# Kernel optimization log

Hardware: AMD Instinct MI355X
Metric: run time of the kernel (lower is better)

The kernel has to match this reference:

```python
import jax, jax.numpy as jnp
import numpy as np

N = 100000   # nodes (batched molecular graphs)
E = 400000   # directed edges
D = 300      # hidden_dim (GNN default)
L = 3        # depth


def setup_inputs() -> dict:
    key = jax.random.key(0)
    ks = jax.random.split(key, 32)
    w = lambda k, s: (jax.random.normal(k, s, dtype=jnp.float32) * 0.05)
    inp = {
        "x": jax.random.normal(ks[0], (N, D), dtype=jnp.float32),
        "edge_attr": jax.random.normal(ks[1], (E, D), dtype=jnp.float32),
        "edge_index": jax.random.randint(ks[2], (2, E), 0, N),
        "W_edge": w(ks[3], (L, D, D)), "b_edge": w(ks[4], (L, D)),
        "W_in":  w(ks[5], (L, D, D)),  # node_in Linear, bias=False
        "W_out": w(ks[6], (L, D, D)),  # node_out Linear, bias=False
        "W_em1": w(ks[7], (L, D, D)),  "b_em1": w(ks[8], (L, D)),
        "W_em2": w(ks[9], (L, D, D)),  "b_em2": w(ks[10], (L, D)),
        "W_n1a": w(ks[11], (L, D, D)), "b_n1a": w(ks[12], (L, D)),
        "W_n1b": w(ks[13], (L, D, D)), "b_n1b": w(ks[14], (L, D)),
        "W_n2a": w(ks[15], (L, D, D)), "b_n2a": w(ks[16], (L, D)),
        "W_n2b": w(ks[17], (L, D, D)), "b_n2b": w(ks[18], (L, D)),
        "edge_eps": jnp.zeros((L,), jnp.float32),  # nn.Parameter([0]) per layer
        "node_eps": jnp.zeros((L,), jnp.float32),
    }
    return inp


def _mlp1(h, Wa, ba, Wb, bb):
    # MLP(num_layers=1): Linear -> ReLU -> Linear
    return jax.nn.relu(h @ Wa + ba) @ Wb + bb


def reference(x, edge_attr, edge_index, W_edge, b_edge, W_in, W_out,
              W_em1, b_em1, W_em2, b_em2, W_n1a, b_n1a, W_n1b, b_n1b,
              W_n2a, b_n2a, W_n2b, b_n2b, edge_eps, node_eps):
    row, col = edge_index[0], edge_index[1]
    n = x.shape[0]
    for l in range(W_edge.shape[0]):
        # EdgeModel: gather endpoints, fused add + relu, then MLP
        f_ij = edge_attr @ W_edge[l] + b_edge[l]          # [E, D]
        f_i = (x @ W_in[l])[row]                           # [E, D] gather
        f_j = (x @ W_out[l])[col]                          # [E, D] gather
        e_msg = _mlp1(jax.nn.relu(f_ij + f_i + f_j),
                      W_em1[l], b_em1[l], W_em2[l], b_em2[l])
        edge_attr = (1.0 + edge_eps[l]) * edge_attr + e_msg
        # NodeModel: edge MLP, scatter_sum to nodes, node MLP
        m = _mlp1(edge_attr, W_n1a[l], b_n1a[l], W_n1b[l], b_n1b[l])
        agg = jax.ops.segment_sum(m, col, num_segments=n)  # [N, D]
        upd = _mlp1(agg, W_n2a[l], b_n2a[l], W_n2b[l], b_n2b[l])
        x = (1.0 + node_eps[l]) * x + upd
    return x, edge_attr
```

## Files before the change

kernel.cpp:

```cpp
#include <hip/hip_runtime.h>

#define NN 100000
#define EE 400000
#define DD 300
#define KP 320
#define LDA 328

typedef __bf16 bf16x8 __attribute__((ext_vector_type(8)));
typedef __bf16 bf16x4 __attribute__((ext_vector_type(4)));
typedef float  floatx4 __attribute__((ext_vector_type(4)));

struct WPtrs { const float* w[27]; };

__global__ void k_prep_weights(WPtrs p, __bf16* __restrict__ wt) {
  __shared__ float tile[64][65];
  const float* W = p.w[blockIdx.z];
  __bf16* out = wt + (size_t)blockIdx.z * (KP * KP);
  const int kb = blockIdx.x * 64, nb = blockIdx.y * 64;
  for (int i = threadIdx.x; i < 64 * 64; i += 256) {
    int tx = i & 63, ty = i >> 6;
    int k = kb + ty, n = nb + tx;
    tile[ty][tx] = (k < DD && n < DD) ? W[k * DD + n] : 0.f;
  }
  __syncthreads();
  for (int i = threadIdx.x; i < 64 * 64; i += 256) {
    int tx = i & 63, ty = i >> 6;
    out[(size_t)(nb + ty) * KP + (kb + tx)] = (__bf16)tile[tx][ty];
  }
}

__device__ __forceinline__ void stage_A64(const float* __restrict__ A, int m0,
                                          int limit, __bf16* lds) {
  for (int i = threadIdx.x; i < 64 * 75; i += 256) {
    int r = i / 75, c4 = (i % 75) * 4;
    bf16x4 b;
    if (m0 + r < limit) {
      float4 v = *(const float4*)(A + (size_t)(m0 + r) * DD + c4);
      b[0] = (__bf16)v.x; b[1] = (__bf16)v.y; b[2] = (__bf16)v.z; b[3] = (__bf16)v.w;
    } else {
      b[0] = (__bf16)0.f; b[1] = (__bf16)0.f; b[2] = (__bf16)0.f; b[3] = (__bf16)0.f;
    }
    *(bf16x4*)(lds + r * LDA + c4) = b;
  }
  for (int i = threadIdx.x; i < 64 * (LDA - DD); i += 256) {
    int r = i / (LDA - DD), c = DD + i % (LDA - DD);
    lds[r * LDA + c] = (__bf16)0.f;
  }
}

__device__ __forceinline__ void gemm64(const __bf16* Alds,
                                       const __bf16* __restrict__ Wt,
                                       int colbase, int quad, int nloc,
                                       floatx4 acc[4][5]) {
#pragma unroll 2
  for (int ks = 0; ks < 10; ++ks) {
    const int k0 = ks * 32 + quad * 8;
    bf16x8 b[5];
#pragma unroll
    for (int t = 0; t < 5; ++t)
      b[t] = *(const bf16x8*)(Wt + (size_t)(colbase + t * 16 + nloc) * KP + k0);
#pragma unroll
    for (int mi = 0; mi < 4; ++mi) {
      bf16x8 a = *(const bf16x8*)(Alds + (mi * 16 + nloc) * LDA + k0);
#pragma unroll
      for (int t = 0; t < 5; ++t)
        acc[mi][t] = __builtin_amdgcn_mfma_f32_16x16x32_bf16(a, b[t], acc[mi][t], 0, 0, 0);
    }
  }
}

#define WAVE64_SETUP                                               \
  const int lane = threadIdx.x & 63, wave = threadIdx.x >> 6;      \
  const int colbase = wave * 80;                                   \
  const int quad = lane >> 4, nloc = lane & 15;                    \
  (void)lane;

#define ZERO_ACC                                                   \
  _Pragma("unroll") for (int mi = 0; mi < 4; ++mi)                 \
  _Pragma("unroll") for (int t = 0; t < 5; ++t)                    \
    acc[mi][t] = (floatx4){0.f, 0.f, 0.f, 0.f};

__global__ __launch_bounds__(256, 3) void k_node_proj(
    const float* __restrict__ x,
    const __bf16* __restrict__ WtA, const __bf16* __restrict__ WtB,
    __bf16* __restrict__ outA, __bf16* __restrict__ outB) {
  __shared__ __attribute__((aligned(16))) __bf16 Alds[64 * LDA];
  const int m0 = blockIdx.x * 64;
  stage_A64(x, m0, NN, Alds);
  __syncthreads();
  WAVE64_SETUP
  floatx4 acc[4][5];
  ZERO_ACC
  gemm64(Alds, WtA, colbase, quad, nloc, acc);
#pragma unroll
  for (int mi = 0; mi < 4; ++mi)
#pragma unroll
    for (int t = 0; t < 5; ++t) {
      const int n = colbase + t * 16 + nloc;
#pragma unroll
      for (int r = 0; r < 4; ++r) {
        const int row = mi * 16 + quad * 4 + r;
        if (m0 + row < NN)
          outA[(size_t)(m0 + row) * KP + n] = (__bf16)acc[mi][t][r];
      }
    }
  ZERO_ACC
  gemm64(Alds, WtB, colbase, quad, nloc, acc);
#pragma unroll
  for (int mi = 0; mi < 4; ++mi)
#pragma unroll
    for (int t = 0; t < 5; ++t) {
      const int n = colbase + t * 16 + nloc;
#pragma unroll
      for (int r = 0; r < 4; ++r) {
        const int row = mi * 16 + quad * 4 + r;
        if (m0 + row < NN)
          outB[(size_t)(m0 + row) * KP + n] = (__bf16)acc[mi][t][r];
      }
    }
}

__global__ __launch_bounds__(256, 3) void k_edge_all(
    float* __restrict__ ea, const int* __restrict__ eidx,
    const __bf16* __restrict__ xin_b, const __bf16* __restrict__ xout_b,
    const __bf16* __restrict__ Wt_e, const float* __restrict__ b_e,
    const __bf16* __restrict__ Wt_1, const float* __restrict__ b_1,
    const __bf16* __restrict__ Wt_2, const float* __restrict__ b_2,
    const __bf16* __restrict__ Wt_a, const float* __restrict__ b_a,
    const __bf16* __restrict__ Wt_b, const float* __restrict__ b_b,
    const float* __restrict__ eps_p, float* __restrict__ agg) {
  __shared__ __attribute__((aligned(16))) __bf16 Alds[64 * LDA];
  __shared__ int ridx[64], cidx[64];
  const int m0 = blockIdx.x * 64;
  stage_A64(ea, m0, EE, Alds);
  if (threadIdx.x < 64) {
    ridx[threadIdx.x] = eidx[m0 + threadIdx.x];
    cidx[threadIdx.x] = eidx[EE + m0 + threadIdx.x];
  }
  __syncthreads();
  WAVE64_SETUP
  floatx4 acc[4][5];

  ZERO_ACC
  gemm64(Alds, Wt_e, colbase, quad, nloc, acc);
  __syncthreads();
#pragma unroll
  for (int mi = 0; mi < 4; ++mi)
#pragma unroll
    for (int t = 0; t < 5; ++t) {
      const int n = colbase + t * 16 + nloc;
      const float bias = (n < DD) ? b_e[n] : 0.f;
#pragma unroll
      for (int r = 0; r < 4; ++r) {
        const int row = mi * 16 + quad * 4 + r;
        const float xi = (float)xin_b[(size_t)ridx[row] * KP + n];
        const float xj = (float)xout_b[(size_t)cidx[row] * KP + n];
        Alds[row * LDA + n] = (__bf16)fmaxf(acc[mi][t][r] + bias + xi + xj, 0.f);
      }
    }
  __syncthreads();

  ZERO_ACC
  gemm64(Alds, Wt_1, colbase, quad, nloc, acc);
  __syncthreads();
#pragma unroll
  for (int mi = 0; mi < 4; ++mi)
#pragma unroll
    for (int t = 0; t < 5; ++t) {
      const int n = colbase + t * 16 + nloc;
      const float bias = (n < DD) ? b_1[n] : 0.f;
#pragma unroll
      for (int r = 0; r < 4; ++r) {
        const int row = mi * 16 + quad * 4 + r;
        Alds[row * LDA + n] = (__bf16)fmaxf(acc[mi][t][r] + bias, 0.f);
      }
    }
  __syncthreads();

  ZERO_ACC
  gemm64(Alds, Wt_2, colbase, quad, nloc, acc);
  __syncthreads();
  const float ep = 1.f + eps_p[0];
#pragma unroll
  for (int mi = 0; mi < 4; ++mi)
#pragma unroll
    for (int t = 0; t < 5; ++t) {
      const int n = colbase + t * 16 + nloc;
#pragma unroll
      for (int r = 0; r < 4; ++r) {
        const int row = mi * 16 + quad * 4 + r;
        float v = 0.f;
        if (n < DD) {
          const size_t off = (size_t)(m0 + row) * DD + n;
          v = ep * ea[off] + acc[mi][t][r] + b_2[n];
          ea[off] = v;
        }
        Alds[row * LDA + n] = (__bf16)v;
      }
    }
  __syncthreads();

  ZERO_ACC
  gemm64(Alds, Wt_a, colbase, quad, nloc, acc);
  __syncthreads();
#pragma unroll
  for (int mi = 0; mi < 4; ++mi)
#pragma unroll
    for (int t = 0; t < 5; ++t) {
      const int n = colbase + t * 16 + nloc;
      const float bias = (n < DD) ? b_a[n] : 0.f;
#pragma unroll
      for (int r = 0; r < 4; ++r) {
        const int row = mi * 16 + quad * 4 + r;
        Alds[row * LDA + n] = (__bf16)fmaxf(acc[mi][t][r] + bias, 0.f);
      }
    }
  __syncthreads();

  ZERO_ACC
  gemm64(Alds, Wt_b, colbase, quad, nloc, acc);
#pragma unroll
  for (int mi = 0; mi < 4; ++mi)
#pragma unroll
    for (int t = 0; t < 5; ++t) {
      const int n = colbase + t * 16 + nloc;
      if (n >= DD) continue;
      const float bias = b_b[n];
#pragma unroll
      for (int r = 0; r < 4; ++r) {
        const int row = mi * 16 + quad * 4 + r;
        unsafeAtomicAdd(&agg[(size_t)cidx[row] * DD + n], acc[mi][t][r] + bias);
      }
    }
}

__global__ __launch_bounds__(256, 3) void k_node_upd(
    const float* __restrict__ agg,
    const __bf16* __restrict__ Wt_a, const float* __restrict__ b_a,
    const __bf16* __restrict__ Wt_b, const float* __restrict__ b_b,
    float* __restrict__ x, const float* __restrict__ eps_p) {
  __shared__ __attribute__((aligned(16))) __bf16 Alds[64 * LDA];
  const int m0 = blockIdx.x * 64;
  stage_A64(agg, m0, NN, Alds);
  __syncthreads();
  WAVE64_SETUP
  floatx4 acc[4][5];
  ZERO_ACC
  gemm64(Alds, Wt_a, colbase, quad, nloc, acc);
  __syncthreads();
#pragma unroll
  for (int mi = 0; mi < 4; ++mi)
#pragma unroll
    for (int t = 0; t < 5; ++t) {
      const int n = colbase + t * 16 + nloc;
      const float bias = (n < DD) ? b_a[n] : 0.f;
#pragma unroll
      for (int r = 0; r < 4; ++r) {
        const int row = mi * 16 + quad * 4 + r;
        Alds[row * LDA + n] = (__bf16)fmaxf(acc[mi][t][r] + bias, 0.f);
      }
    }
  __syncthreads();
  ZERO_ACC
  gemm64(Alds, Wt_b, colbase, quad, nloc, acc);
  const float ep = 1.f + eps_p[0];
#pragma unroll
  for (int mi = 0; mi < 4; ++mi)
#pragma unroll
    for (int t = 0; t < 5; ++t) {
      const int n = colbase + t * 16 + nloc;
      if (n >= DD) continue;
      const float bias = b_b[n];
#pragma unroll
      for (int r = 0; r < 4; ++r) {
        const int row = mi * 16 + quad * 4 + r;
        if (m0 + row < NN) {
          const size_t off = (size_t)(m0 + row) * DD + n;
          x[off] = ep * x[off] + acc[mi][t][r] + bias;
        }
      }
    }
}

extern "C" void kernel_launch(void* const* d_in, const int* in_sizes, int n_in,
                              void* d_out, int out_size, void* d_ws, size_t ws_size,
                              hipStream_t stream) {
  const float* x_in   = (const float*)d_in[0];
  const float* ea_in  = (const float*)d_in[1];
  const int*   eidx   = (const int*)d_in[2];
  const float* W_edge = (const float*)d_in[3];
  const float* b_edge = (const float*)d_in[4];
  const float* W_in   = (const float*)d_in[5];
  const float* W_out  = (const float*)d_in[6];
  const float* W_em1  = (const float*)d_in[7];
  const float* b_em1  = (const float*)d_in[8];
  const float* W_em2  = (const float*)d_in[9];
  const float* b_em2  = (const float*)d_in[10];
  const float* W_n1a  = (const float*)d_in[11];
  const float* b_n1a  = (const float*)d_in[12];
  const float* W_n1b  = (const float*)d_in[13];
  const float* b_n1b  = (const float*)d_in[14];
  const float* W_n2a  = (const float*)d_in[15];
  const float* b_n2a  = (const float*)d_in[16];
  const float* W_n2b  = (const float*)d_in[17];
  const float* b_n2b  = (const float*)d_in[18];
  const float* e_eps  = (const float*)d_in[19];
  const float* n_eps  = (const float*)d_in[20];

  float* x  = (float*)d_out;
  float* ea = (float*)d_out + (size_t)NN * DD;

  char* ws = (char*)d_ws;
  __bf16* Wt     = (__bf16*)ws;
  __bf16* xin_b  = (__bf16*)(ws + 5529600);
  __bf16* xout_b = (__bf16*)(ws + 5529600 + 64000000);
  float*  agg    = (float*)(ws + 5529600 + 128000000);

  hipMemcpyAsync(x,  x_in,  (size_t)NN * DD * 4, hipMemcpyDeviceToDevice, stream);
  hipMemcpyAsync(ea, ea_in, (size_t)EE * DD * 4, hipMemcpyDeviceToDevice, stream);

  WPtrs wp;
  for (int l = 0; l < 3; ++l) {
    const size_t o = (size_t)l * DD * DD;
    wp.w[l*9 + 0] = W_edge + o; wp.w[l*9 + 1] = W_in  + o; wp.w[l*9 + 2] = W_out + o;
    wp.w[l*9 + 3] = W_em1 + o;  wp.w[l*9 + 4] = W_em2 + o;
    wp.w[l*9 + 5] = W_n1a + o;  wp.w[l*9 + 6] = W_n1b + o;
    wp.w[l*9 + 7] = W_n2a + o;  wp.w[l*9 + 8] = W_n2b + o;
  }
  k_prep_weights<<<dim3(5, 5, 27), 256, 0, stream>>>(wp, Wt);

  const int nblk_node = (NN + 63) / 64;
  const int nblk_edge = EE / 64;

  for (int l = 0; l < 3; ++l) {
    const __bf16* wt = Wt + (size_t)l * 9 * KP * KP;
    const size_t bo = (size_t)l * DD;
    k_node_proj<<<nblk_node, 256, 0, stream>>>(x, wt + 1 * KP * KP, wt + 2 * KP * KP,
                                               xin_b, xout_b);
    hipMemsetAsync(agg, 0, (size_t)NN * DD * 4, stream);
    k_edge_all<<<nblk_edge, 256, 0, stream>>>(ea, eidx, xin_b, xout_b,
        wt + 0 * KP * KP, b_edge + bo,
        wt + 3 * KP * KP, b_em1 + bo,
        wt + 4 * KP * KP, b_em2 + bo,
        wt + 5 * KP * KP, b_n1a + bo,
        wt + 6 * KP * KP, b_n1b + bo,
        e_eps + l, agg);
    k_node_upd<<<nblk_node, 256, 0, stream>>>(agg,
        wt + 7 * KP * KP, b_n2a + bo,
        wt + 8 * KP * KP, b_n2b + bo, x, n_eps + l);
  }
}
```

Before: 6.519 ms.

## Use 8 waves per block with 2x4 tile split and vectorized endpoint gather

Blocks grow from 4 to 8 waves. Each wave now computes a 32-row by 80-column tile instead of 64 rows by 80 columns, which halves the accumulator registers per wave and raises occupancy. The per-element scalar gathers of xin/xout in the first edge epilogue are replaced by a separate pass that does 16-byte bf16x8 loads of whole rows and fuses them with the pre-activation held in LDS. The trade-off is that each wave reloads weight fragments for fewer MFMAs, so weight traffic from L2 per block roughly doubles, and the new pass adds an extra LDS round trip and a barrier.

```diff
diff --git a/kernel.cpp b/kernel.cpp
--- a/kernel.cpp
+++ b/kernel.cpp
@@ -31,7 +31,7 @@
 
 __device__ __forceinline__ void stage_A64(const float* __restrict__ A, int m0,
                                           int limit, __bf16* lds) {
-  for (int i = threadIdx.x; i < 64 * 75; i += 256) {
+  for (int i = threadIdx.x; i < 64 * 75; i += 512) {
     int r = i / 75, c4 = (i % 75) * 4;
     bf16x4 b;
     if (m0 + r < limit) {
@@ -42,17 +42,16 @@
     }
     *(bf16x4*)(lds + r * LDA + c4) = b;
   }
-  for (int i = threadIdx.x; i < 64 * (LDA - DD); i += 256) {
+  for (int i = threadIdx.x; i < 64 * (LDA - DD); i += 512) {
     int r = i / (LDA - DD), c = DD + i % (LDA - DD);
     lds[r * LDA + c] = (__bf16)0.f;
   }
 }
 
-__device__ __forceinline__ void gemm64(const __bf16* Alds,
+__device__ __forceinline__ void gemm8w(const __bf16* Alds,
                                        const __bf16* __restrict__ Wt,
-                                       int colbase, int quad, int nloc,
-                                       floatx4 acc[4][5]) {
-#pragma unroll 2
+                                       int rowbase, int colbase, int quad, int nloc,
+                                       floatx4 acc[2][5]) {
   for (int ks = 0; ks < 10; ++ks) {
     const int k0 = ks * 32 + quad * 8;
     bf16x8 b[5];
@@ -60,8 +59,8 @@
     for (int t = 0; t < 5; ++t)
       b[t] = *(const bf16x8*)(Wt + (size_t)(colbase + t * 16 + nloc) * KP + k0);
 #pragma unroll
-    for (int mi = 0; mi < 4; ++mi) {
-      bf16x8 a = *(const bf16x8*)(Alds + (mi * 16 + nloc) * LDA + k0);
+    for (int mi = 0; mi < 2; ++mi) {
+      bf16x8 a = *(const bf16x8*)(Alds + (rowbase + mi * 16 + nloc) * LDA + k0);
 #pragma unroll
       for (int t = 0; t < 5; ++t)
         acc[mi][t] = __builtin_amdgcn_mfma_f32_16x16x32_bf16(a, b[t], acc[mi][t], 0, 0, 0);
@@ -69,18 +68,18 @@
   }
 }
 
-#define WAVE64_SETUP                                               \
+#define WAVE8_SETUP                                                \
   const int lane = threadIdx.x & 63, wave = threadIdx.x >> 6;      \
-  const int colbase = wave * 80;                                   \
+  const int rowbase = (wave & 1) * 32, colbase = (wave >> 1) * 80; \
   const int quad = lane >> 4, nloc = lane & 15;                    \
   (void)lane;
 
 #define ZERO_ACC                                                   \
-  _Pragma("unroll") for (int mi = 0; mi < 4; ++mi)                 \
+  _Pragma("unroll") for (int mi = 0; mi < 2; ++mi)                 \
   _Pragma("unroll") for (int t = 0; t < 5; ++t)                    \
     acc[mi][t] = (floatx4){0.f, 0.f, 0.f, 0.f};
 
-__global__ __launch_bounds__(256, 3) void k_node_proj(
+__global__ __launch_bounds__(512, 6) void k_node_proj(
     const float* __restrict__ x,
     const __bf16* __restrict__ WtA, const __bf16* __restrict__ WtB,
     __bf16* __restrict__ outA, __bf16* __restrict__ outB) {
@@ -88,39 +87,39 @@
   const int m0 = blockIdx.x * 64;
   stage_A64(x, m0, NN, Alds);
   __syncthreads();
-  WAVE64_SETUP
-  floatx4 acc[4][5];
-  ZERO_ACC
-  gemm64(Alds, WtA, colbase, quad, nloc, acc);
-#pragma unroll
-  for (int mi = 0; mi < 4; ++mi)
-#pragma unroll
-    for (int t = 0; t < 5; ++t) {
-      const int n = colbase + t * 16 + nloc;
-#pragma unroll
-      for (int r = 0; r < 4; ++r) {
-        const int row = mi * 16 + quad * 4 + r;
+  WAVE8_SETUP
+  floatx4 acc[2][5];
+  ZERO_ACC
+  gemm8w(Alds, WtA, rowbase, colbase, quad, nloc, acc);
+#pragma unroll
+  for (int mi = 0; mi < 2; ++mi)
+#pragma unroll
+    for (int t = 0; t < 5; ++t) {
+      const int n = colbase + t * 16 + nloc;
+#pragma unroll
+      for (int r = 0; r < 4; ++r) {
+        const int row = rowbase + mi * 16 + quad * 4 + r;
         if (m0 + row < NN)
           outA[(size_t)(m0 + row) * KP + n] = (__bf16)acc[mi][t][r];
       }
     }
   ZERO_ACC
-  gemm64(Alds, WtB, colbase, quad, nloc, acc);
-#pragma unroll
-  for (int mi = 0; mi < 4; ++mi)
-#pragma unroll
-    for (int t = 0; t < 5; ++t) {
-      const int n = colbase + t * 16 + nloc;
-#pragma unroll
-      for (int r = 0; r < 4; ++r) {
-        const int row = mi * 16 + quad * 4 + r;
+  gemm8w(Alds, WtB, rowbase, colbase, quad, nloc, acc);
+#pragma unroll
+  for (int mi = 0; mi < 2; ++mi)
+#pragma unroll
+    for (int t = 0; t < 5; ++t) {
+      const int n = colbase + t * 16 + nloc;
+#pragma unroll
+      for (int r = 0; r < 4; ++r) {
+        const int row = rowbase + mi * 16 + quad * 4 + r;
         if (m0 + row < NN)
           outB[(size_t)(m0 + row) * KP + n] = (__bf16)acc[mi][t][r];
       }
     }
 }
 
-__global__ __launch_bounds__(256, 3) void k_edge_all(
+__global__ __launch_bounds__(512, 6) void k_edge_all(
     float* __restrict__ ea, const int* __restrict__ eidx,
     const __bf16* __restrict__ xin_b, const __bf16* __restrict__ xout_b,
     const __bf16* __restrict__ Wt_e, const float* __restrict__ b_e,
@@ -138,57 +137,67 @@
     cidx[threadIdx.x] = eidx[EE + m0 + threadIdx.x];
   }
   __syncthreads();
-  WAVE64_SETUP
-  floatx4 acc[4][5];
-
-  ZERO_ACC
-  gemm64(Alds, Wt_e, colbase, quad, nloc, acc);
-  __syncthreads();
-#pragma unroll
-  for (int mi = 0; mi < 4; ++mi)
+  WAVE8_SETUP
+  floatx4 acc[2][5];
+
+  ZERO_ACC
+  gemm8w(Alds, Wt_e, rowbase, colbase, quad, nloc, acc);
+  __syncthreads();
+#pragma unroll
+  for (int mi = 0; mi < 2; ++mi)
 #pragma unroll
     for (int t = 0; t < 5; ++t) {
       const int n = colbase + t * 16 + nloc;
       const float bias = (n < DD) ? b_e[n] : 0.f;
 #pragma unroll
       for (int r = 0; r < 4; ++r) {
-        const int row = mi * 16 + quad * 4 + r;
-        const float xi = (float)xin_b[(size_t)ridx[row] * KP + n];
-        const float xj = (float)xout_b[(size_t)cidx[row] * KP + n];
-        Alds[row * LDA + n] = (__bf16)fmaxf(acc[mi][t][r] + bias + xi + xj, 0.f);
-      }
-    }
-  __syncthreads();
-
-  ZERO_ACC
-  gemm64(Alds, Wt_1, colbase, quad, nloc, acc);
-  __syncthreads();
-#pragma unroll
-  for (int mi = 0; mi < 4; ++mi)
+        const int row = rowbase + mi * 16 + quad * 4 + r;
+        Alds[row * LDA + n] = (__bf16)(acc[mi][t][r] + bias);
+      }
+    }
+  __syncthreads();
+  for (int i = threadIdx.x; i < 64 * 40; i += 512) {
+    const int row = i / 40, c8 = (i % 40) * 8;
+    bf16x8 p  = *(const bf16x8*)(Alds + row * LDA + c8);
+    bf16x8 xi = *(const bf16x8*)(xin_b  + (size_t)ridx[row] * KP + c8);
+    bf16x8 xj = *(const bf16x8*)(xout_b + (size_t)cidx[row] * KP + c8);
+    bf16x8 h;
+#pragma unroll
+    for (int j = 0; j < 8; ++j)
+      h[j] = (__bf16)fmaxf((float)p[j] + (float)xi[j] + (float)xj[j], 0.f);
+    *(bf16x8*)(Alds + row * LDA + c8) = h;
+  }
+  __syncthreads();
+
+  ZERO_ACC
+  gemm8w(Alds, Wt_1, rowbase, colbase, quad, nloc, acc);
+  __syncthreads();
+#pragma unroll
+  for (int mi = 0; mi < 2; ++mi)
 #pragma unroll
     for (int t = 0; t < 5; ++t) {
       const int n = colbase + t * 16 + nloc;
       const float bias = (n < DD) ? b_1[n] : 0.f;
 #pragma unroll
       for (int r = 0; r < 4; ++r) {
-        const int row = mi * 16 + quad * 4 + r;
+        const int row = rowbase + mi * 16 + quad * 4 + r;
         Alds[row * LDA + n] = (__bf16)fmaxf(acc[mi][t][r] + bias, 0.f);
       }
     }
   __syncthreads();
 
   ZERO_ACC
-  gemm64(Alds, Wt_2, colbase, quad, nloc, acc);
+  gemm8w(Alds, Wt_2, rowbase, colbase, quad, nloc, acc);
   __syncthreads();
   const float ep = 1.f + eps_p[0];
 #pragma unroll
-  for (int mi = 0; mi < 4; ++mi)
-#pragma unroll
-    for (int t = 0; t < 5; ++t) {
-      const int n = colbase + t * 16 + nloc;
-#pragma unroll
-      for (int r = 0; r < 4; ++r) {
-        const int row = mi * 16 + quad * 4 + r;
+  for (int mi = 0; mi < 2; ++mi)
+#pragma unroll
+    for (int t = 0; t < 5; ++t) {
+      const int n = colbase + t * 16 + nloc;
+#pragma unroll
+      for (int r = 0; r < 4; ++r) {
+        const int row = rowbase + mi * 16 + quad * 4 + r;
         float v = 0.f;
         if (n < DD) {
           const size_t off = (size_t)(m0 + row) * DD + n;
@@ -201,26 +210,26 @@
   __syncthreads();
 
   ZERO_ACC
-  gemm64(Alds, Wt_a, colbase, quad, nloc, acc);
-  __syncthreads();
-#pragma unroll
-  for (int mi = 0; mi < 4; ++mi)
+  gemm8w(Alds, Wt_a, rowbase, colbase, quad, nloc, acc);
+  __syncthreads();
+#pragma unroll
+  for (int mi = 0; mi < 2; ++mi)
 #pragma unroll
     for (int t = 0; t < 5; ++t) {
       const int n = colbase + t * 16 + nloc;
       const float bias = (n < DD) ? b_a[n] : 0.f;
 #pragma unroll
       for (int r = 0; r < 4; ++r) {
-        const int row = mi * 16 + quad * 4 + r;
+        const int row = rowbase + mi * 16 + quad * 4 + r;
         Alds[row * LDA + n] = (__bf16)fmaxf(acc[mi][t][r] + bias, 0.f);
       }
     }
   __syncthreads();
 
   ZERO_ACC
-  gemm64(Alds, Wt_b, colbase, quad, nloc, acc);
-#pragma unroll
-  for (int mi = 0; mi < 4; ++mi)
+  gemm8w(Alds, Wt_b, rowbase, colbase, quad, nloc, acc);
+#pragma unroll
+  for (int mi = 0; mi < 2; ++mi)
 #pragma unroll
     for (int t = 0; t < 5; ++t) {
       const int n = colbase + t * 16 + nloc;
@@ -228,13 +237,13 @@
       const float bias = b_b[n];
 #pragma unroll
       for (int r = 0; r < 4; ++r) {
-        const int row = mi * 16 + quad * 4 + r;
+        const int row = rowbase + mi * 16 + quad * 4 + r;
         unsafeAtomicAdd(&agg[(size_t)cidx[row] * DD + n], acc[mi][t][r] + bias);
       }
     }
 }
 
-__global__ __launch_bounds__(256, 3) void k_node_upd(
+__global__ __launch_bounds__(512, 6) void k_node_upd(
     const float* __restrict__ agg,
     const __bf16* __restrict__ Wt_a, const float* __restrict__ b_a,
     const __bf16* __restrict__ Wt_b, const float* __restrict__ b_b,
@@ -243,29 +252,29 @@
   const int m0 = blockIdx.x * 64;
   stage_A64(agg, m0, NN, Alds);
   __syncthreads();
-  WAVE64_SETUP
-  floatx4 acc[4][5];
-  ZERO_ACC
-  gemm64(Alds, Wt_a, colbase, quad, nloc, acc);
-  __syncthreads();
-#pragma unroll
-  for (int mi = 0; mi < 4; ++mi)
+  WAVE8_SETUP
+  floatx4 acc[2][5];
+  ZERO_ACC
+  gemm8w(Alds, Wt_a, rowbase, colbase, quad, nloc, acc);
+  __syncthreads();
+#pragma unroll
+  for (int mi = 0; mi < 2; ++mi)
 #pragma unroll
     for (int t = 0; t < 5; ++t) {
       const int n = colbase + t * 16 + nloc;
       const float bias = (n < DD) ? b_a[n] : 0.f;
 #pragma unroll
       for (int r = 0; r < 4; ++r) {
-        const int row = mi * 16 + quad * 4 + r;
+        const int row = rowbase + mi * 16 + quad * 4 + r;
         Alds[row * LDA + n] = (__bf16)fmaxf(acc[mi][t][r] + bias, 0.f);
       }
     }
   __syncthreads();
   ZERO_ACC
-  gemm64(Alds, Wt_b, colbase, quad, nloc, acc);
+  gemm8w(Alds, Wt_b, rowbase, colbase, quad, nloc, acc);
   const float ep = 1.f + eps_p[0];
 #pragma unroll
-  for (int mi = 0; mi < 4; ++mi)
+  for (int mi = 0; mi < 2; ++mi)
 #pragma unroll
     for (int t = 0; t < 5; ++t) {
       const int n = colbase + t * 16 + nloc;
@@ -273,7 +282,7 @@
       const float bias = b_b[n];
 #pragma unroll
       for (int r = 0; r < 4; ++r) {
-        const int row = mi * 16 + quad * 4 + r;
+        const int row = rowbase + mi * 16 + quad * 4 + r;
         if (m0 + row < NN) {
           const size_t off = (size_t)(m0 + row) * DD + n;
           x[off] = ep * x[off] + acc[mi][t][r] + bias;
@@ -335,17 +344,17 @@
   for (int l = 0; l < 3; ++l) {
     const __bf16* wt = Wt + (size_t)l * 9 * KP * KP;
     const size_t bo = (size_t)l * DD;
-    k_node_proj<<<nblk_node, 256, 0, stream>>>(x, wt + 1 * KP * KP, wt + 2 * KP * KP,
+    k_node_proj<<<nblk_node, 512, 0, stream>>>(x, wt + 1 * KP * KP, wt + 2 * KP * KP,
                                                xin_b, xout_b);
     hipMemsetAsync(agg, 0, (size_t)NN * DD * 4, stream);
-    k_edge_all<<<nblk_edge, 256, 0, stream>>>(ea, eidx, xin_b, xout_b,
+    k_edge_all<<<nblk_edge, 512, 0, stream>>>(ea, eidx, xin_b, xout_b,
         wt + 0 * KP * KP, b_edge + bo,
         wt + 3 * KP * KP, b_em1 + bo,
         wt + 4 * KP * KP, b_em2 + bo,
         wt + 5 * KP * KP, b_n1a + bo,
         wt + 6 * KP * KP, b_n1b + bo,
         e_eps + l, agg);
-    k_node_upd<<<nblk_node, 256, 0, stream>>>(agg,
+    k_node_upd<<<nblk_node, 512, 0, stream>>>(agg,
         wt + 7 * KP * KP, b_n2a + bo,
         wt + 8 * KP * KP, b_n2b + bo, x, n_eps + l);
   }
```

After: 9.973 ms. +53.0%, slower.
